# Performance work log

Hardware: AMD Instinct MI355X
Metric: run time of the kernel (lower is better)

Reference implementation:

```python
import jax, jax.numpy as jnp
import numpy as np

D = 400   # d_model
H = 16    # num heads
KD = 400  # keras MHA key_dim (per-head dim)
GU = 1800 # GRU units
EPS = 1e-6


def _ln(x, g, b):
    m = jnp.mean(x, -1, keepdims=True)
    v = jnp.mean((x - m) ** 2, -1, keepdims=True)
    return (x - m) * jax.lax.rsqrt(v + EPS) * g + b


def _gru_step(x, K, RK, B):
    # Single timestep keras GRU (reset_after=True, activation=elu, h0=0).
    h0 = jnp.zeros((x.shape[0], RK.shape[0]), x.dtype)
    xz, xr, xh = jnp.split(x @ K + B[0], 3, axis=-1)
    rz, rr, rh = jnp.split(h0 @ RK + B[1], 3, axis=-1)
    z = jax.nn.sigmoid(xz + rz)
    r = jax.nn.sigmoid(xr + rr)
    hh = jax.nn.elu(xh + r * rh)
    return z * h0 + (1.0 - z) * hh


def _forward(x, Wq, bq, Wk, bk, Wv, bv, Wo, bo, ln1_g, ln1_b,
             ffn_w1, ffn_b1, ffn_w2, ffn_b2, ln2_g, ln2_b,
             gru_fk, gru_frk, gru_fb, gru_bk, gru_brk, gru_bb,
             d2_w, d2_b, d4_w, d4_b, out_w, out_b):
    # The original python loop over growing prefixes is equivalent to one
    # batched encoder pass over inputs[1:, -1:, :] (seq_len==1, so MHA is
    # per-batch-element independent), with the raw row inputs[0] prepended.
    xe = x[1:, -1:, :]  # [N-1, 1, D]
    q = jnp.einsum('bsd,dhk->bshk', xe, Wq) + bq
    k = jnp.einsum('bsd,dhk->bshk', xe, Wk) + bk
    v = jnp.einsum('bsd,dhk->bshk', xe, Wv) + bv
    logits = jnp.einsum('bqhk,bmhk->bhqm', q, k) / jnp.sqrt(jnp.float32(KD))
    probs = jax.nn.softmax(logits, axis=-1)  # trivially ones (seq=1)
    ctx = jnp.einsum('bhqm,bmhk->bqhk', probs, v)
    attn = jnp.einsum('bqhk,hkd->bqd', ctx, Wo) + bo
    out1 = _ln(xe + attn, ln1_g, ln1_b)
    ffn = jax.nn.relu(out1 @ ffn_w1 + ffn_b1) @ ffn_w2 + ffn_b2
    enc = _ln(out1 + ffn, ln2_g, ln2_b)  # [N-1, 1, D]
    output = jnp.concatenate([x[:1, -1:, :], enc], axis=0)  # [N, 1, D]
    upd = jnp.concatenate([x, output], axis=1)              # [N, 4, D]
    flat = upd.reshape(x.shape[0], -1)                      # [N, 1600]
    # frozen cite_cos_sim_model (inference: dropout layers are identity)
    hf = _gru_step(flat, gru_fk, gru_frk, gru_fb)
    hb = _gru_step(flat, gru_bk, gru_brk, gru_bb)
    x1 = jnp.concatenate([hf, hb], axis=-1)   # [N, 3600]
    x3 = jax.nn.elu(x1 @ d2_w + d2_b)         # [N, 1800]
    x5 = jax.nn.elu(x3 @ d4_w + d4_b)         # [N, 1800]
    cat = jnp.concatenate([x1, x3, x5], axis=-1)  # [N, 7200]
    return cat @ out_w + out_b                # [N, 140]


def setup_inputs() -> dict:
    key = jax.random.key(0)
    shapes = {
        'Wq': (D, H, KD), 'bq': (H, KD), 'Wk': (D, H, KD), 'bk': (H, KD),
        'Wv': (D, H, KD), 'bv': (H, KD), 'Wo': (H, KD, D), 'bo': (D,),
        'ln1_b': (D,), 'ffn_w1': (D, 2), 'ffn_b1': (2,), 'ffn_w2': (2, D),
        'ffn_b2': (D,), 'ln2_b': (D,),
        'gru_fk': (1600, 3 * GU), 'gru_frk': (GU, 3 * GU), 'gru_fb': (2, 3 * GU),
        'gru_bk': (1600, 3 * GU), 'gru_brk': (GU, 3 * GU), 'gru_bb': (2, 3 * GU),
        'd2_w': (2 * GU, GU), 'd2_b': (GU,), 'd4_w': (GU, GU), 'd4_b': (GU,),
        'out_w': (4 * GU, 140), 'out_b': (140,),
    }
    keys = jax.random.split(key, len(shapes) + 1)
    inp = {'x': jax.random.normal(keys[0], (16384, 3, D), jnp.float32)}
    for i, (name, sh) in enumerate(shapes.items()):
        inp[name] = jax.random.normal(keys[i + 1], sh, jnp.float32) * 0.02
    inp['ln1_g'] = jnp.ones((D,), jnp.float32)
    inp['ln2_g'] = jnp.ones((D,), jnp.float32)
    return inp


def reference(x, Wq, bq, Wk, bk, Wv, bv, Wo, bo, ln1_g, ln1_b,
              ffn_w1, ffn_b1, ffn_w2, ffn_b2, ln2_g, ln2_b,
              gru_fk, gru_frk, gru_fb, gru_bk, gru_brk, gru_bb,
              d2_w, d2_b, d4_w, d4_b, out_w, out_b):
    return _forward(x, Wq, bq, Wk, bk, Wv, bv, Wo, bo, ln1_g, ln1_b,
                    ffn_w1, ffn_b1, ffn_w2, ffn_b2, ln2_g, ln2_b,
                    gru_fk, gru_frk, gru_fb, gru_bk, gru_brk, gru_bb,
                    d2_w, d2_b, d4_w, d4_b, out_w, out_b)
```

## Files before the change

### kernel.cpp

```cpp
#include <hip/hip_runtime.h>
#include <hip/hip_bf16.h>

typedef unsigned short u16;
using bf16x8 = __attribute__((ext_vector_type(8))) short;
using f32x4  = __attribute__((ext_vector_type(4))) float;

#define CM 2048
#define NC 8

#define P_LN1G 0
#define P_LN1B 400
#define P_FW1  800
#define P_FB1  1600
#define P_FW2  1602
#define P_FB2  2402
#define P_LN2G 2802
#define P_LN2B 3202
#define P_GFB  3602
#define P_GBB  14402
#define P_BV   25202
#define P_BO   31602
#define P_OB   32002
#define P_END  32142

__device__ __forceinline__ u16 f2bf(float f) {
  unsigned u = __float_as_uint(f);
  unsigned r = u + 0x7FFFu + ((u >> 16) & 1u);
  return (u16)(r >> 16);
}
__device__ __forceinline__ float bf2f(u16 h) {
  return __uint_as_float(((unsigned)h) << 16);
}

__device__ __forceinline__ void gl_lds16(const u16* g, u16* l) {
  __builtin_amdgcn_global_load_lds(
      (__attribute__((address_space(1))) void*)g,
      (__attribute__((address_space(3))) void*)l, 16, 0, 0);
}

__global__ void detect_dtype(int* flag, const void* x) {
  if (threadIdx.x == 0 && blockIdx.x == 0) {
    const u16* p = (const u16*)x;
    int cnt = 0;
    for (int i = 0; i < 64; i++) {
      int e = (p[2 * i] >> 7) & 0xFF;
      if (e >= 0x70 && e <= 0x85) cnt++;
    }
    *flag = (cnt >= 32) ? 1 : 0;
  }
}

__global__ void canon_bf(u16* __restrict__ dst, const void* __restrict__ src,
                         int n, const int* __restrict__ flag) {
  int i = blockIdx.x * 256 + threadIdx.x;
  if (i >= n) return;
  dst[i] = (*flag) ? ((const u16*)src)[i] : f2bf(((const float*)src)[i]);
}

__global__ void canon_x_rows(u16* __restrict__ dst, const void* __restrict__ src,
                             long base, int n, const int* __restrict__ flag) {
  int i = blockIdx.x * 256 + threadIdx.x;
  if (i >= n) return;
  long j = base + i;
  dst[i] = (*flag) ? ((const u16*)src)[j] : f2bf(((const float*)src)[j]);
}

__global__ void canon_f32k(float* __restrict__ dst, const void* __restrict__ src,
                           int n, const int* __restrict__ flag) {
  int i = blockIdx.x * 256 + threadIdx.x;
  if (i >= n) return;
  dst[i] = (*flag) ? bf2f(((const u16*)src)[i]) : ((const float*)src)[i];
}

__global__ void f32_to_bf(u16* __restrict__ dst, const float* __restrict__ src, int n) {
  int i = blockIdx.x * 256 + threadIdx.x;
  if (i < n) dst[i] = f2bf(src[i]);
}

template <int EPI, bool CL>
__global__ __launch_bounds__(256) void gemm_bt(
    const u16* __restrict__ A, const u16* __restrict__ Bt, void* __restrict__ Cv,
    const float* __restrict__ bias, int M, int N, int K, int lda, int ldb, int ldc,
    const u16* aend)
{
  __shared__ u16 lsA[128 * 32];
  __shared__ u16 lsB[128 * 32];
  const int tid = threadIdx.x;
  const int m0 = blockIdx.x * 128, n0 = blockIdx.y * 128;
  const int wave = tid >> 6, lane = tid & 63;
  const int wm = (wave >> 1) << 6, wn = (wave & 1) << 6;
  const int quad = lane >> 4, l16 = lane & 15;

  int ra = m0 + (tid >> 2);       if (ra > M - 1) ra = M - 1;
  int ra2 = m0 + 64 + (tid >> 2); if (ra2 > M - 1) ra2 = M - 1;
  int rb = n0 + (tid >> 2);       if (rb > N - 1) rb = N - 1;
  int rb2 = n0 + 64 + (tid >> 2); if (rb2 > N - 1) rb2 = N - 1;
  const u16* Ag  = A + (size_t)ra * lda + (tid & 3) * 8;
  const u16* Ag2 = A + (size_t)ra2 * lda + (tid & 3) * 8;
  const u16* Bg  = Bt + (size_t)rb * ldb + (tid & 3) * 8;
  const u16* Bg2 = Bt + (size_t)rb2 * ldb + (tid & 3) * 8;
  u16* la = lsA + tid * 8;
  u16* lb = lsB + tid * 8;

  f32x4 acc[4][4];
#pragma unroll
  for (int i = 0; i < 4; i++)
#pragma unroll
    for (int j = 0; j < 4; j++) acc[i][j] = (f32x4){0.f, 0.f, 0.f, 0.f};

  for (int k0 = 0; k0 < K; k0 += 32) {
    __syncthreads();
    const u16* pa  = Ag + k0;
    const u16* pa2 = Ag2 + k0;
    if (CL) { if (pa > aend) pa = aend; if (pa2 > aend) pa2 = aend; }
    gl_lds16(pa, la);
    gl_lds16(pa2, la + 2048);
    gl_lds16(Bg + k0, lb);
    gl_lds16(Bg2 + k0, lb + 2048);
    __syncthreads();
    bf16x8 af[4], bfv[4];
#pragma unroll
    for (int t = 0; t < 4; t++) {
      af[t]  = *(const bf16x8*)(lsA + ((wm + t * 16 + l16) << 5) + (quad << 3));
      bfv[t] = *(const bf16x8*)(lsB + ((wn + t * 16 + l16) << 5) + (quad << 3));
    }
#pragma unroll
    for (int mt = 0; mt < 4; mt++)
#pragma unroll
      for (int nt = 0; nt < 4; nt++)
        acc[mt][nt] = __builtin_amdgcn_mfma_f32_16x16x32_bf16(af[mt], bfv[nt], acc[mt][nt], 0, 0, 0);
  }

#pragma unroll
  for (int mt = 0; mt < 4; mt++)
#pragma unroll
    for (int r = 0; r < 4; r++) {
      const int row = m0 + wm + mt * 16 + quad * 4 + r;
      if (row < M) {
#pragma unroll
        for (int nt = 0; nt < 4; nt++) {
          const int col = n0 + wn + nt * 16 + l16;
          if (col < N) {
            float v = acc[mt][nt][r];
            if (EPI == 0) ((u16*)Cv)[(size_t)row * ldc + col] = f2bf(v);
            if (EPI == 1) ((float*)Cv)[(size_t)row * ldc + col] = v + bias[col];
            if (EPI == 2) {
              float p = v + bias[col];
              ((u16*)Cv)[(size_t)row * ldc + col] = f2bf(p > 0.f ? p : expm1f(p));
            }
          }
        }
      }
    }
}

template <int EPI>
__global__ __launch_bounds__(512, 2) void gemm256_bt(
    const u16* __restrict__ A, const u16* __restrict__ Bt, void* __restrict__ Cv,
    const float* __restrict__ bias, int M, int N, int K, int lda, int ldb, int ldc)
{
  __shared__ u16 lds8[65536];
  const int tid = threadIdx.x;
  const int m0 = blockIdx.x * 256, n0 = blockIdx.y * 256;
  const int wave = tid >> 6, lane = tid & 63;
  const int wm = (wave >> 2) * 128;
  const int wn = (wave & 3) * 64;
  const int quad = lane >> 4, l16 = lane & 15;

  const int srow = tid >> 3;
  const int sblk = ((tid & 7) ^ (srow & 7)) * 8;
  const u16* Ag[4];
  const u16* Bg[4];
#pragma unroll
  for (int i = 0; i < 4; i++) {
    int raw = m0 + i * 64 + srow; if (raw > M - 1) raw = M - 1;
    int rbw = n0 + i * 64 + srow; if (rbw > N - 1) rbw = N - 1;
    Ag[i] = A  + (size_t)raw * lda + sblk;
    Bg[i] = Bt + (size_t)rbw * ldb + sblk;
  }

  f32x4 acc[8][4];
#pragma unroll
  for (int i = 0; i < 8; i++)
#pragma unroll
    for (int j = 0; j < 4; j++) acc[i][j] = (f32x4){0.f, 0.f, 0.f, 0.f};

  const int nT = K >> 6;
#pragma unroll
  for (int i = 0; i < 4; i++) gl_lds16(Ag[i], lds8 + i * 4096 + tid * 8);
#pragma unroll
  for (int i = 0; i < 4; i++) gl_lds16(Bg[i], lds8 + 16384 + i * 4096 + tid * 8);

  int c = 0;
  for (int t = 0; t < nT; ++t) {
    __builtin_amdgcn_s_barrier();
    if (t + 1 < nT) {
      const int k1 = (t + 1) << 6;
      u16* dst = lds8 + (c ^ 1) * 32768;
#pragma unroll
      for (int i = 0; i < 4; i++) gl_lds16(Ag[i] + k1, dst + i * 4096 + tid * 8);
#pragma unroll
      for (int i = 0; i < 4; i++) gl_lds16(Bg[i] + k1, dst + 16384 + i * 4096 + tid * 8);
      asm volatile("s_waitcnt vmcnt(8)" ::: "memory");
    } else {
      asm volatile("s_waitcnt vmcnt(0)" ::: "memory");
    }
    __builtin_amdgcn_s_barrier();
    const u16* lA = lds8 + c * 32768;
    const u16* lB = lA + 16384;
#pragma unroll
    for (int kk = 0; kk < 2; kk++) {
      const int ch = kk * 4 + quad;
      bf16x8 af[8], bv[4];
#pragma unroll
      for (int mt = 0; mt < 8; mt++)
        af[mt] = *(const bf16x8*)(lA + (wm + mt * 16 + l16) * 64 + ((ch ^ (l16 & 7)) * 8));
#pragma unroll
      for (int nt = 0; nt < 4; nt++)
        bv[nt] = *(const bf16x8*)(lB + (wn + nt * 16 + l16) * 64 + ((ch ^ (l16 & 7)) * 8));
      __builtin_amdgcn_s_setprio(1);
#pragma unroll
      for (int mt = 0; mt < 8; mt++)
#pragma unroll
        for (int nt = 0; nt < 4; nt++)
          acc[mt][nt] = __builtin_amdgcn_mfma_f32_16x16x32_bf16(af[mt], bv[nt], acc[mt][nt], 0, 0, 0);
      __builtin_amdgcn_s_setprio(0);
    }
    c ^= 1;
  }

#pragma unroll
  for (int mt = 0; mt < 8; mt++)
#pragma unroll
    for (int r = 0; r < 4; r++) {
      const int row = m0 + wm + mt * 16 + quad * 4 + r;
      if (row < M) {
#pragma unroll
        for (int nt = 0; nt < 4; nt++) {
          const int col = n0 + wn + nt * 16 + l16;
          if (col < N) {
            float v = acc[mt][nt][r];
            if (EPI == 0) ((u16*)Cv)[(size_t)row * ldc + col] = f2bf(v);
            if (EPI == 2) {
              float p = v + bias[col];
              ((u16*)Cv)[(size_t)row * ldc + col] = f2bf(p > 0.f ? p : expm1f(p));
            }
          }
        }
      }
    }
}

__global__ __launch_bounds__(256) void gemm_bt_sk(
    const u16* __restrict__ A, const u16* __restrict__ Bt, float* __restrict__ outf,
    int M, int N, int K, int lda, int ldb, int ldc)
{
  __shared__ u16 lsA[128 * 32];
  __shared__ u16 lsB[128 * 32];
  const int tid = threadIdx.x;
  const int m0 = blockIdx.x * 128, n0 = blockIdx.y * 128;
  const int wave = tid >> 6, lane = tid & 63;
  const int wm = (wave >> 1) << 6, wn = (wave & 1) << 6;
  const int quad = lane >> 4, l16 = lane & 15;
  const int S = K >> 5, kz = blockIdx.z, KS = gridDim.z;
  const int s0 = (S * kz) / KS, s1 = (S * (kz + 1)) / KS;

  int ra = m0 + (tid >> 2);       if (ra > M - 1) ra = M - 1;
  int ra2 = m0 + 64 + (tid >> 2); if (ra2 > M - 1) ra2 = M - 1;
  int rb = n0 + (tid >> 2);       if (rb > N - 1) rb = N - 1;
  int rb2 = n0 + 64 + (tid >> 2); if (rb2 > N - 1) rb2 = N - 1;
  const u16* Ag  = A + (size_t)ra * lda + (tid & 3) * 8;
  const u16* Ag2 = A + (size_t)ra2 * lda + (tid & 3) * 8;
  const u16* Bg  = Bt + (size_t)rb * ldb + (tid & 3) * 8;
  const u16* Bg2 = Bt + (size_t)rb2 * ldb + (tid & 3) * 8;
  u16* la = lsA + tid * 8;
  u16* lb = lsB + tid * 8;

  f32x4 acc[4][4];
#pragma unroll
  for (int i = 0; i < 4; i++)
#pragma unroll
    for (int j = 0; j < 4; j++) acc[i][j] = (f32x4){0.f, 0.f, 0.f, 0.f};

  for (int s = s0; s < s1; ++s) {
    const int k0 = s << 5;
    __syncthreads();
    gl_lds16(Ag + k0, la);
    gl_lds16(Ag2 + k0, la + 2048);
    gl_lds16(Bg + k0, lb);
    gl_lds16(Bg2 + k0, lb + 2048);
    __syncthreads();
    bf16x8 af[4], bfv[4];
#pragma unroll
    for (int t = 0; t < 4; t++) {
      af[t]  = *(const bf16x8*)(lsA + ((wm + t * 16 + l16) << 5) + (quad << 3));
      bfv[t] = *(const bf16x8*)(lsB + ((wn + t * 16 + l16) << 5) + (quad << 3));
    }
#pragma unroll
    for (int mt = 0; mt < 4; mt++)
#pragma unroll
      for (int nt = 0; nt < 4; nt++)
        acc[mt][nt] = __builtin_amdgcn_mfma_f32_16x16x32_bf16(af[mt], bfv[nt], acc[mt][nt], 0, 0, 0);
  }

#pragma unroll
  for (int mt = 0; mt < 4; mt++)
#pragma unroll
    for (int r = 0; r < 4; r++) {
      const int row = m0 + wm + mt * 16 + quad * 4 + r;
      if (row < M) {
#pragma unroll
        for (int nt = 0; nt < 4; nt++) {
          const int col = n0 + wn + nt * 16 + l16;
          if (col < N) atomicAdd(&outf[(size_t)row * ldc + col], acc[mt][nt][r]);
        }
      }
    }
}

__global__ __launch_bounds__(256) void transpose_bf(
    u16* __restrict__ dst, const void* __restrict__ src, int SR, int SC, int DR, int DC,
    const int* __restrict__ flag)
{
  __shared__ u16 t[32][33];
  const int fl = *flag;
  const int tx = threadIdx.x & 31, ty = threadIdx.x >> 5;
  const int j0 = blockIdx.x << 5;
  const int i0 = blockIdx.y << 5;
#pragma unroll
  for (int s = 0; s < 32; s += 8) {
    int sr = j0 + ty + s, sc = i0 + tx;
    u16 v = 0;
    if (sr < SR && sc < SC) {
      size_t idx = (size_t)sr * SC + sc;
      v = fl ? ((const u16*)src)[idx] : f2bf(((const float*)src)[idx]);
    }
    t[ty + s][tx] = v;
  }
  __syncthreads();
#pragma unroll
  for (int s = 0; s < 32; s += 8) {
    int dr = i0 + ty + s, dc = j0 + tx;
    if (dr < DR && dc < DC) dst[(size_t)dr * DC + dc] = t[tx][ty + s];
  }
}

__global__ void build_outT(u16* __restrict__ dst, const void* __restrict__ ow,
                           const int* __restrict__ flag) {
  const int fl = *flag;
  int idx = blockIdx.x * 256 + threadIdx.x;
  if (idx >= 140 * 7264) return;
  int o = idx / 7264, c = idx - o * 7264;
  long si = -1;
  if (c < 3600) si = (long)c * 140 + o;
  else if (c >= 3616 && c < 5416) si = (long)(c - 16) * 140 + o;
  else if (c >= 5440 && c < 7240) si = (long)(c - 40) * 140 + o;
  u16 v = 0;
  if (si >= 0) v = fl ? ((const u16*)ow)[si] : f2bf(((const float*)ow)[si]);
  dst[idx] = v;
}

__global__ void zero_u32(unsigned* p, int n) {
  int i = blockIdx.x * 256 + threadIdx.x;
  if (i < n) p[i] = 0;
}

__global__ void zero_catpads(u16* cat, int rows) {
  int idx = blockIdx.x * 256 + threadIdx.x;
  if (idx >= rows * 64) return;
  int b = idx >> 6, t = idx & 63;
  int col = t < 16 ? 3600 + t : (t < 40 ? 5400 + t : 7200 + t);
  cat[(size_t)b * 7264 + col] = 0;
}

__global__ void init_outf(float* __restrict__ outf, const u16* __restrict__ pbuf) {
  int i = blockIdx.x * 256 + threadIdx.x;
  if (i < 16384 * 140) outf[i] = bf2f(pbuf[P_OB + i % 140]);
}

__device__ __forceinline__ void block_sum2(float& a, float& b, float* red, int t) {
#pragma unroll
  for (int o = 32; o > 0; o >>= 1) { a += __shfl_down(a, o, 64); b += __shfl_down(b, o, 64); }
  __syncthreads();
  if ((t & 63) == 0) { red[t >> 6] = a; red[4 + (t >> 6)] = b; }
  __syncthreads();
  a = red[0] + red[1] + red[2] + red[3];
  b = red[4] + red[5] + red[6] + red[7];
}

__global__ __launch_bounds__(256) void c0_kernel(float* c0, const u16* __restrict__ WoT,
                                                 const u16* __restrict__ pbuf) {
  __shared__ float red[8];
  int d = blockIdx.x, t = threadIdx.x;
  const u16* row = WoT + (size_t)d * 6400;
  const u16* bv = pbuf + P_BV;
  float s = 0.f;
  for (int j = t; j < 6400; j += 256) s += bf2f(bv[j]) * bf2f(row[j]);
  float dummy = 0.f;
  block_sum2(s, dummy, red, t);
  if (t == 0) c0[d] = s + bf2f(pbuf[P_BO + d]);
}

__global__ __launch_bounds__(256) void enc_rows(
    const u16* __restrict__ xc, const float* __restrict__ attn,
    const u16* __restrict__ pbuf, u16* __restrict__ flatc, int r0)
{
  __shared__ float red[8];
  const int li = blockIdx.x, t = threadIdx.x;
  const int gr = r0 + li;
  const u16* xr = xc + (size_t)li * 1200;
  u16* fr = flatc + (size_t)li * 1600;
  if (t < 150) ((uint4*)fr)[t] = ((const uint4*)xr)[t];
  if (gr == 0) {
    if (t < 50) ((uint4*)(fr + 1200))[t] = ((const uint4*)(xr + 800))[t];
    return;
  }
  const u16* xe = xr + 800;
  const float* at = attn + (size_t)li * 400;
  const u16 *g1 = pbuf + P_LN1G, *b1 = pbuf + P_LN1B, *fw1 = pbuf + P_FW1,
            *fb1v = pbuf + P_FB1, *fw2 = pbuf + P_FW2, *fb2v = pbuf + P_FB2,
            *g2 = pbuf + P_LN2G, *b2 = pbuf + P_LN2B;
  const int i1 = t + 256;
  float a0 = bf2f(xe[t]) + at[t];
  float a1 = 0.f;
  if (i1 < 400) a1 = bf2f(xe[i1]) + at[i1];
  float s = a0 + a1, ss = a0 * a0 + a1 * a1;
  block_sum2(s, ss, red, t);
  float mean = s * (1.f / 400.f);
  float var = ss * (1.f / 400.f) - mean * mean;
  float rstd = rsqrtf(var + 1e-6f);
  float o0 = (a0 - mean) * rstd * bf2f(g1[t]) + bf2f(b1[t]);
  float o1 = 0.f;
  if (i1 < 400) o1 = (a1 - mean) * rstd * bf2f(g1[i1]) + bf2f(b1[i1]);
  float d0 = o0 * bf2f(fw1[2 * t]), d1 = o0 * bf2f(fw1[2 * t + 1]);
  if (i1 < 400) { d0 += o1 * bf2f(fw1[2 * i1]); d1 += o1 * bf2f(fw1[2 * i1 + 1]); }
  block_sum2(d0, d1, red, t);
  float t0 = d0 + bf2f(fb1v[0]); t0 = t0 > 0.f ? t0 : 0.f;
  float t1 = d1 + bf2f(fb1v[1]); t1 = t1 > 0.f ? t1 : 0.f;
  float c0v = o0 + t0 * bf2f(fw2[t]) + t1 * bf2f(fw2[400 + t]) + bf2f(fb2v[t]);
  float c1v = 0.f;
  if (i1 < 400) c1v = o1 + t0 * bf2f(fw2[i1]) + t1 * bf2f(fw2[400 + i1]) + bf2f(fb2v[i1]);
  s = c0v + c1v; ss = c0v * c0v + c1v * c1v;
  block_sum2(s, ss, red, t);
  mean = s * (1.f / 400.f);
  var = ss * (1.f / 400.f) - mean * mean;
  rstd = rsqrtf(var + 1e-6f);
  u16* dr = fr + 1200;
  dr[t] = f2bf((c0v - mean) * rstd * bf2f(g2[t]) + bf2f(b2[t]));
  if (i1 < 400) dr[i1] = f2bf((c1v - mean) * rstd * bf2f(g2[i1]) + bf2f(b2[i1]));
}

__global__ __launch_bounds__(256) void gru_act(
    const u16* __restrict__ G, int ldg, const u16* __restrict__ pbuf, int boff,
    u16* __restrict__ cat, int off, int rows)
{
  int idx = blockIdx.x * 256 + threadIdx.x;
  if (idx >= rows * 1800) return;
  int b = idx / 1800, u = idx - b * 1800;
  const u16* g = G + (size_t)b * ldg;
  const u16* B = pbuf + boff;
  float xz = bf2f(g[u]) + bf2f(B[u]) + bf2f(B[5400 + u]);
  float xr = bf2f(g[1800 + u]) + bf2f(B[1800 + u]) + bf2f(B[7200 + u]);
  float xh = bf2f(g[3600 + u]) + bf2f(B[3600 + u]);
  float rh = bf2f(B[9000 + u]);
  float z = 1.f / (1.f + expf(-xz));
  float r = 1.f / (1.f + expf(-xr));
  float pre = xh + r * rh;
  float hh = pre > 0.f ? pre : expm1f(pre);
  cat[(size_t)b * 7264 + off + u] = f2bf((1.f - z) * hh);
}

extern "C" void kernel_launch(void* const* d_in, const int* in_sizes, int n_in,
                              void* d_out, int out_size, void* d_ws, size_t ws_size,
                              hipStream_t stream) {
  static const int MAP_DICT[22] = {5,6,7,8, 9,10,11,12,13,14, 15,17,18,20, 21,22,23,24, 25,26, 27,28};
  static const int MAP_SIG[22]  = {5,6,7,8, 10,11,12,13,14,16, 17,19,20,22, 23,24,25,26, 27,28, 9,15};
  const int* MAP = (in_sizes[15] > 100000) ? MAP_DICT : MAP_SIG;

  const void* x    = d_in[0];
  const void* Wv   = d_in[MAP[0]];
  const void* bv   = d_in[MAP[1]];
  const void* Wo   = d_in[MAP[2]];
  const void* bo   = d_in[MAP[3]];
  const void* ln1b = d_in[MAP[4]];
  const void* fw1  = d_in[MAP[5]];
  const void* fb1  = d_in[MAP[6]];
  const void* fw2  = d_in[MAP[7]];
  const void* fb2  = d_in[MAP[8]];
  const void* ln2b = d_in[MAP[9]];
  const void* gfk  = d_in[MAP[10]];
  const void* gfb  = d_in[MAP[11]];
  const void* gbk  = d_in[MAP[12]];
  const void* gbb  = d_in[MAP[13]];
  const void* d2w  = d_in[MAP[14]];
  const void* d2b  = d_in[MAP[15]];
  const void* d4w  = d_in[MAP[16]];
  const void* d4b  = d_in[MAP[17]];
  const void* ow   = d_in[MAP[18]];
  const void* ob   = d_in[MAP[19]];
  const void* ln1g = d_in[MAP[20]];
  const void* ln2g = d_in[MAP[21]];
  float* outf = (float*)d_out;

  unsigned char* base = (unsigned char*)d_ws;
  size_t off = 0;
  auto take = [&](size_t bytes) -> void* {
    void* p = base + off;
    off += (bytes + 255) & ~(size_t)255;
    return p;
  };
  u16*   KfT   = (u16*)take((size_t)5400 * 1600 * 2);
  u16*   KbT   = (u16*)take((size_t)5400 * 1600 * 2);
  u16*   d2T   = (u16*)take((size_t)1800 * 3616 * 2);
  u16*   d4T   = (u16*)take((size_t)1800 * 1824 * 2);
  u16*   outT  = (u16*)take((size_t)140 * 7264 * 2);
  u16*   WoT   = (u16*)take((size_t)400 * 6400 * 2);
  u16*   MT    = (u16*)take((size_t)400 * 416 * 2);
  float* MTf   = (float*)take((size_t)400 * 416 * 4);
  u16*   pbuf  = (u16*)take((size_t)P_END * 2);
  int*   flag  = (int*)take(256);
  float* c0    = (float*)take(400 * 4);
  float* d2bf  = (float*)take(1800 * 4);
  float* d4bf  = (float*)take(1800 * 4);

  int CMV = 0;
  {
    const size_t avail  = ws_size > off ? ws_size - off : 0;
    const size_t perrow = (size_t)(1600 + 10800 + 7264) * 2;
    const size_t margin = (size_t)4 << 20;
    if      (avail >= (size_t)16384 * perrow + margin) CMV = 16384;
    else if (avail >= (size_t)8192  * perrow + margin) CMV = 8192;
    else if (avail >= (size_t)4096  * perrow + margin) CMV = 4096;
    else if (avail >= (size_t)2048  * perrow + margin) CMV = 2048;
  }

  u16 *flatc, *Gc, *catc;
  if (CMV) {
    flatc = (u16*)take((size_t)CMV * 1600 * 2);
    Gc    = (u16*)take((size_t)CMV * 10800 * 2);
    catc  = (u16*)take((size_t)CMV * 7264 * 2);
  } else {
    flatc = (u16*)take((size_t)CM * 1600 * 2);
    Gc    = (u16*)take((size_t)CM * 5400 * 2);
    catc  = (u16*)take((size_t)CM * 7264 * 2);
  }
  const int rows = CMV ? CMV : CM;
  float* attnc = (float*)Gc;
  u16*   xc    = (u16*)((unsigned char*)Gc + (size_t)rows * 1600);
  u16*   Wvc   = catc;

  detect_dtype<<<1, 64, 0, stream>>>(flag, x);
  canon_bf<<<2, 256, 0, stream>>>(pbuf + P_LN1G, ln1g, 400, flag);
  canon_bf<<<2, 256, 0, stream>>>(pbuf + P_LN1B, ln1b, 400, flag);
  canon_bf<<<4, 256, 0, stream>>>(pbuf + P_FW1, fw1, 800, flag);
  canon_bf<<<1, 256, 0, stream>>>(pbuf + P_FB1, fb1, 2, flag);
  canon_bf<<<4, 256, 0, stream>>>(pbuf + P_FW2, fw2, 800, flag);
  canon_bf<<<2, 256, 0, stream>>>(pbuf + P_FB2, fb2, 400, flag);
  canon_bf<<<2, 256, 0, stream>>>(pbuf + P_LN2G, ln2g, 400, flag);
  canon_bf<<<2, 256, 0, stream>>>(pbuf + P_LN2B, ln2b, 400, flag);
  canon_bf<<<43, 256, 0, stream>>>(pbuf + P_GFB, gfb, 10800, flag);
  canon_bf<<<43, 256, 0, stream>>>(pbuf + P_GBB, gbb, 10800, flag);
  canon_bf<<<25, 256, 0, stream>>>(pbuf + P_BV, bv, 6400, flag);
  canon_bf<<<2, 256, 0, stream>>>(pbuf + P_BO, bo, 400, flag);
  canon_bf<<<1, 256, 0, stream>>>(pbuf + P_OB, ob, 140, flag);
  canon_f32k<<<8, 256, 0, stream>>>(d2bf, d2b, 1800, flag);
  canon_f32k<<<8, 256, 0, stream>>>(d4bf, d4b, 1800, flag);

  transpose_bf<<<dim3(50, 169), 256, 0, stream>>>(KfT, gfk, 1600, 5400, 5400, 1600, flag);
  transpose_bf<<<dim3(50, 169), 256, 0, stream>>>(KbT, gbk, 1600, 5400, 5400, 1600, flag);
  transpose_bf<<<dim3(113, 57), 256, 0, stream>>>(d2T, d2w, 3600, 1800, 1800, 3616, flag);
  transpose_bf<<<dim3(57, 57), 256, 0, stream>>>(d4T, d4w, 1800, 1800, 1800, 1824, flag);
  transpose_bf<<<dim3(200, 13), 256, 0, stream>>>(WoT, Wo, 6400, 400, 400, 6400, flag);
  build_outT<<<(140 * 7264 + 255) / 256, 256, 0, stream>>>(outT, ow, flag);
  init_outf<<<(16384 * 140 + 255) / 256, 256, 0, stream>>>(outf, pbuf);
  c0_kernel<<<400, 256, 0, stream>>>(c0, WoT, pbuf);

  canon_bf<<<10000, 256, 0, stream>>>(Wvc, Wv, 2560000, flag);
  zero_u32<<<(166400 + 255) / 256, 256, 0, stream>>>((unsigned*)MTf, 166400);
  gemm_bt_sk<<<dim3(4, 4, 16), 256, 0, stream>>>(WoT, Wvc, MTf,
      400, 400, 6400, 6400, 6400, 416);
  f32_to_bf<<<(166400 + 255) / 256, 256, 0, stream>>>(MT, MTf, 166400);

  if (CMV) {
    zero_catpads<<<(CMV * 64 + 255) / 256, 256, 0, stream>>>(catc, CMV);
    const int nchunk = 16384 / CMV;
    for (int c = 0; c < nchunk; ++c) {
      const long r0 = (long)c * CMV;
      canon_x_rows<<<(CMV * 1200 + 255) / 256, 256, 0, stream>>>(
          xc, x, r0 * 1200, CMV * 1200, flag);
      gemm_bt<1, true><<<dim3(CMV / 128, 4), 256, 0, stream>>>(
          xc + 800, MT, attnc, c0, CMV, 400, 416, 1200, 416, 400,
          xc + (size_t)CMV * 1200 - 8);
      enc_rows<<<CMV, 256, 0, stream>>>(xc, attnc, pbuf, flatc, (int)r0);
      gemm256_bt<0><<<dim3(CMV / 256, 43), 512, 0, stream>>>(
          flatc, KfT, Gc, nullptr, CMV, 10800, 1600, 1600, 1600, 10800);
      gru_act<<<(CMV * 1800 + 255) / 256, 256, 0, stream>>>(
          Gc, 10800, pbuf, P_GFB, catc, 0, CMV);
      gru_act<<<(CMV * 1800 + 255) / 256, 256, 0, stream>>>(
          Gc + 5400, 10800, pbuf, P_GBB, catc, 1800, CMV);
      gemm_bt<2, false><<<dim3(CMV / 128, 15), 256, 0, stream>>>(
          catc, d2T, catc + 3616, d2bf, CMV, 1800, 3616, 7264, 3616, 7264, nullptr);
      gemm_bt<2, false><<<dim3(CMV / 128, 15), 256, 0, stream>>>(
          catc + 3616, d4T, catc + 5440, d4bf, CMV, 1800, 1824, 7264, 1824, 7264, nullptr);
      gemm_bt_sk<<<dim3(CMV / 128, 2, 8), 256, 0, stream>>>(
          catc, outT, outf + (size_t)r0 * 140, CMV, 140, 7264, 7264, 7264, 140);
    }
  } else {
    zero_catpads<<<(CM * 64 + 255) / 256, 256, 0, stream>>>(catc, CM);
    for (int c = 0; c < NC; ++c) {
      const int r0 = c * CM;
      canon_x_rows<<<(CM * 1200 + 255) / 256, 256, 0, stream>>>(
          xc, x, (long)r0 * 1200, CM * 1200, flag);
      gemm_bt<1, true><<<dim3(CM / 128, 4), 256, 0, stream>>>(
          xc + 800, MT, attnc, c0, CM, 400, 416, 1200, 416, 400,
          xc + (size_t)CM * 1200 - 8);
      enc_rows<<<CM, 256, 0, stream>>>(xc, attnc, pbuf, flatc, r0);
      gemm_bt<0, false><<<dim3(CM / 128, 43), 256, 0, stream>>>(
          flatc, KfT, Gc, nullptr, CM, 5400, 1600, 1600, 1600, 5400, nullptr);
      gru_act<<<(CM * 1800 + 255) / 256, 256, 0, stream>>>(
          Gc, 5400, pbuf, P_GFB, catc, 0, CM);
      gemm_bt<0, false><<<dim3(CM / 128, 43), 256, 0, stream>>>(
          flatc, KbT, Gc, nullptr, CM, 5400, 1600, 1600, 1600, 5400, nullptr);
      gru_act<<<(CM * 1800 + 255) / 256, 256, 0, stream>>>(
          Gc, 5400, pbuf, P_GBB, catc, 1800, CM);
      gemm_bt<2, false><<<dim3(CM / 128, 15), 256, 0, stream>>>(
          catc, d2T, catc + 3616, d2bf, CM, 1800, 3616, 7264, 3616, 7264, nullptr);
      gemm_bt<2, false><<<dim3(CM / 128, 15), 256, 0, stream>>>(
          catc + 3616, d4T, catc + 5440, d4bf, CM, 1800, 1824, 7264, 1824, 7264, nullptr);
      gemm_bt_sk<<<dim3(CM / 128, 2, 8), 256, 0, stream>>>(
          catc, outT, outf + (size_t)r0 * 140, CM, 140, 7264, 7264, 7264, 140);
    }
  }
}
```

Baseline: 2.282 ms.

## Deepen GEMM256 pipeline to 4 stages, split-K attention GEMM, fuse GRU activations

The 256x256 GEMM now uses K-tiles of 32 with a four-buffer LDS ring and three tiles prefetched ahead, in place of 64-wide double buffering. The goal is to hide more global-load latency behind MFMA work. The attention projection GEMM becomes a split-K atomic kernel that writes into a bias-initialised fp32 buffer, adding parallelism for that narrow output. The forward and backward GRU activation kernels are merged into a single launch. In exchange there are more barriers per K, an extra init kernel, and atomic accumulation.

```diff
diff --git a/kernel.cpp b/kernel.cpp
--- a/kernel.cpp
+++ b/kernel.cpp
@@ -77,6 +77,12 @@
   if (i < n) dst[i] = f2bf(src[i]);
 }
 
+__global__ void init_bias_f32(float* __restrict__ dst, const float* __restrict__ b,
+                              int p, int n) {
+  int i = blockIdx.x * 256 + threadIdx.x;
+  if (i < n) dst[i] = b[i % p];
+}
+
 template <int EPI, bool CL>
 __global__ __launch_bounds__(256) void gemm_bt(
     const u16* __restrict__ A, const u16* __restrict__ Bt, void* __restrict__ Cv,
@@ -167,14 +173,14 @@
   const int wn = (wave & 3) * 64;
   const int quad = lane >> 4, l16 = lane & 15;
 
-  const int srow = tid >> 3;
-  const int sblk = ((tid & 7) ^ (srow & 7)) * 8;
-  const u16* Ag[4];
-  const u16* Bg[4];
-#pragma unroll
-  for (int i = 0; i < 4; i++) {
-    int raw = m0 + i * 64 + srow; if (raw > M - 1) raw = M - 1;
-    int rbw = n0 + i * 64 + srow; if (rbw > N - 1) rbw = N - 1;
+  const int srow = tid >> 2;
+  const int sblk = ((tid & 3) ^ ((srow >> 1) & 3)) * 8;
+  const u16* Ag[2];
+  const u16* Bg[2];
+#pragma unroll
+  for (int i = 0; i < 2; i++) {
+    int raw = m0 + i * 128 + srow; if (raw > M - 1) raw = M - 1;
+    int rbw = n0 + i * 128 + srow; if (rbw > N - 1) rbw = N - 1;
     Ag[i] = A  + (size_t)raw * lda + sblk;
     Bg[i] = Bt + (size_t)rbw * ldb + sblk;
   }
@@ -185,48 +191,58 @@
 #pragma unroll
     for (int j = 0; j < 4; j++) acc[i][j] = (f32x4){0.f, 0.f, 0.f, 0.f};
 
-  const int nT = K >> 6;
-#pragma unroll
-  for (int i = 0; i < 4; i++) gl_lds16(Ag[i], lds8 + i * 4096 + tid * 8);
-#pragma unroll
-  for (int i = 0; i < 4; i++) gl_lds16(Bg[i], lds8 + 16384 + i * 4096 + tid * 8);
-
-  int c = 0;
+  const int nT = K >> 5;
+#pragma unroll
+  for (int p = 0; p < 3; ++p) {
+    if (p < nT) {
+      u16* dst = lds8 + p * 16384;
+      const int kp = p << 5;
+#pragma unroll
+      for (int i = 0; i < 2; i++) gl_lds16(Ag[i] + kp, dst + i * 4096 + tid * 8);
+#pragma unroll
+      for (int i = 0; i < 2; i++) gl_lds16(Bg[i] + kp, dst + 8192 + i * 4096 + tid * 8);
+    }
+  }
+
   for (int t = 0; t < nT; ++t) {
     __builtin_amdgcn_s_barrier();
-    if (t + 1 < nT) {
-      const int k1 = (t + 1) << 6;
-      u16* dst = lds8 + (c ^ 1) * 32768;
-#pragma unroll
-      for (int i = 0; i < 4; i++) gl_lds16(Ag[i] + k1, dst + i * 4096 + tid * 8);
-#pragma unroll
-      for (int i = 0; i < 4; i++) gl_lds16(Bg[i] + k1, dst + 16384 + i * 4096 + tid * 8);
+    if (t + 3 < nT) {
+      const int k1 = (t + 3) << 5;
+      u16* dst = lds8 + ((t + 3) & 3) * 16384;
+#pragma unroll
+      for (int i = 0; i < 2; i++) gl_lds16(Ag[i] + k1, dst + i * 4096 + tid * 8);
+#pragma unroll
+      for (int i = 0; i < 2; i++) gl_lds16(Bg[i] + k1, dst + 8192 + i * 4096 + tid * 8);
+      asm volatile("s_waitcnt vmcnt(12)" ::: "memory");
+    } else if (t + 2 < nT) {
       asm volatile("s_waitcnt vmcnt(8)" ::: "memory");
+    } else if (t + 1 < nT) {
+      asm volatile("s_waitcnt vmcnt(4)" ::: "memory");
     } else {
       asm volatile("s_waitcnt vmcnt(0)" ::: "memory");
     }
     __builtin_amdgcn_s_barrier();
-    const u16* lA = lds8 + c * 32768;
-    const u16* lB = lA + 16384;
-#pragma unroll
-    for (int kk = 0; kk < 2; kk++) {
-      const int ch = kk * 4 + quad;
-      bf16x8 af[8], bv[4];
-#pragma unroll
-      for (int mt = 0; mt < 8; mt++)
-        af[mt] = *(const bf16x8*)(lA + (wm + mt * 16 + l16) * 64 + ((ch ^ (l16 & 7)) * 8));
+
+    const u16* lA = lds8 + (t & 3) * 16384;
+    const u16* lB = lA + 8192;
+    bf16x8 av[8], bv[4];
+#pragma unroll
+    for (int mt = 0; mt < 8; mt++) {
+      const int row = wm + mt * 16 + l16;
+      av[mt] = *(const bf16x8*)(lA + row * 32 + ((quad ^ ((row >> 1) & 3)) * 8));
+    }
+#pragma unroll
+    for (int nt = 0; nt < 4; nt++) {
+      const int row = wn + nt * 16 + l16;
+      bv[nt] = *(const bf16x8*)(lB + row * 32 + ((quad ^ ((row >> 1) & 3)) * 8));
+    }
+    __builtin_amdgcn_s_setprio(1);
+#pragma unroll
+    for (int mt = 0; mt < 8; mt++)
 #pragma unroll
       for (int nt = 0; nt < 4; nt++)
-        bv[nt] = *(const bf16x8*)(lB + (wn + nt * 16 + l16) * 64 + ((ch ^ (l16 & 7)) * 8));
-      __builtin_amdgcn_s_setprio(1);
-#pragma unroll
-      for (int mt = 0; mt < 8; mt++)
-#pragma unroll
-        for (int nt = 0; nt < 4; nt++)
-          acc[mt][nt] = __builtin_amdgcn_mfma_f32_16x16x32_bf16(af[mt], bv[nt], acc[mt][nt], 0, 0, 0);
-      __builtin_amdgcn_s_setprio(0);
-    }
-    c ^= 1;
+        acc[mt][nt] = __builtin_amdgcn_mfma_f32_16x16x32_bf16(av[mt], bv[nt], acc[mt][nt], 0, 0, 0);
+    __builtin_amdgcn_s_setprio(0);
   }
 
 #pragma unroll
@@ -251,9 +267,10 @@
     }
 }
 
+template <bool CL>
 __global__ __launch_bounds__(256) void gemm_bt_sk(
     const u16* __restrict__ A, const u16* __restrict__ Bt, float* __restrict__ outf,
-    int M, int N, int K, int lda, int ldb, int ldc)
+    int M, int N, int K, int lda, int ldb, int ldc, const u16* aend)
 {
   __shared__ u16 lsA[128 * 32];
   __shared__ u16 lsB[128 * 32];
@@ -285,8 +302,11 @@
   for (int s = s0; s < s1; ++s) {
     const int k0 = s << 5;
     __syncthreads();
-    gl_lds16(Ag + k0, la);
-    gl_lds16(Ag2 + k0, la + 2048);
+    const u16* pa  = Ag + k0;
+    const u16* pa2 = Ag2 + k0;
+    if (CL) { if (pa > aend) pa = aend; if (pa2 > aend) pa2 = aend; }
+    gl_lds16(pa, la);
+    gl_lds16(pa2, la + 2048);
     gl_lds16(Bg + k0, lb);
     gl_lds16(Bg2 + k0, lb + 2048);
     __syncthreads();
@@ -470,6 +490,28 @@
   cat[(size_t)b * 7264 + off + u] = f2bf((1.f - z) * hh);
 }
 
+__global__ __launch_bounds__(256) void gru_act2(
+    const u16* __restrict__ G, const u16* __restrict__ pbuf,
+    u16* __restrict__ cat, int rows)
+{
+  int idx = blockIdx.x * 256 + threadIdx.x;
+  if (idx >= rows * 3600) return;
+  int b = idx / 3600, u2 = idx - b * 3600;
+  const int fwd = u2 < 1800;
+  const int u = fwd ? u2 : u2 - 1800;
+  const u16* g = G + (size_t)b * 10800 + (fwd ? 0 : 5400);
+  const u16* B = pbuf + (fwd ? P_GFB : P_GBB);
+  float xz = bf2f(g[u]) + bf2f(B[u]) + bf2f(B[5400 + u]);
+  float xr = bf2f(g[1800 + u]) + bf2f(B[1800 + u]) + bf2f(B[7200 + u]);
+  float xh = bf2f(g[3600 + u]) + bf2f(B[3600 + u]);
+  float rh = bf2f(B[9000 + u]);
+  float z = 1.f / (1.f + expf(-xz));
+  float r = 1.f / (1.f + expf(-xr));
+  float pre = xh + r * rh;
+  float hh = pre > 0.f ? pre : expm1f(pre);
+  cat[(size_t)b * 7264 + u2] = f2bf((1.f - z) * hh);
+}
+
 extern "C" void kernel_launch(void* const* d_in, const int* in_sizes, int n_in,
                               void* d_out, int out_size, void* d_ws, size_t ws_size,
                               hipStream_t stream) {
@@ -577,8 +619,8 @@
 
   canon_bf<<<10000, 256, 0, stream>>>(Wvc, Wv, 2560000, flag);
   zero_u32<<<(166400 + 255) / 256, 256, 0, stream>>>((unsigned*)MTf, 166400);
-  gemm_bt_sk<<<dim3(4, 4, 16), 256, 0, stream>>>(WoT, Wvc, MTf,
-      400, 400, 6400, 6400, 6400, 416);
+  gemm_bt_sk<false><<<dim3(4, 4, 16), 256, 0, stream>>>(WoT, Wvc, MTf,
+      400, 400, 6400, 6400, 6400, 416, nullptr);
   f32_to_bf<<<(166400 + 255) / 256, 256, 0, stream>>>(MT, MTf, 166400);
 
   if (CMV) {
@@ -588,22 +630,20 @@
       const long r0 = (long)c * CMV;
       canon_x_rows<<<(CMV * 1200 + 255) / 256, 256, 0, stream>>>(
           xc, x, r0 * 1200, CMV * 1200, flag);
-      gemm_bt<1, true><<<dim3(CMV / 128, 4), 256, 0, stream>>>(
-          xc + 800, MT, attnc, c0, CMV, 400, 416, 1200, 416, 400,
+      init_bias_f32<<<(CMV * 400 + 255) / 256, 256, 0, stream>>>(attnc, c0, 400, CMV * 400);
+      gemm_bt_sk<true><<<dim3(CMV / 128, 4, 4), 256, 0, stream>>>(
+          xc + 800, MT, attnc, CMV, 400, 416, 1200, 416, 400,
           xc + (size_t)CMV * 1200 - 8);
       enc_rows<<<CMV, 256, 0, stream>>>(xc, attnc, pbuf, flatc, (int)r0);
       gemm256_bt<0><<<dim3(CMV / 256, 43), 512, 0, stream>>>(
           flatc, KfT, Gc, nullptr, CMV, 10800, 1600, 1600, 1600, 10800);
-      gru_act<<<(CMV * 1800 + 255) / 256, 256, 0, stream>>>(
-          Gc, 10800, pbuf, P_GFB, catc, 0, CMV);
-      gru_act<<<(CMV * 1800 + 255) / 256, 256, 0, stream>>>(
-          Gc + 5400, 10800, pbuf, P_GBB, catc, 1800, CMV);
+      gru_act2<<<(CMV * 3600 + 255) / 256, 256, 0, stream>>>(Gc, pbuf, catc, CMV);
       gemm_bt<2, false><<<dim3(CMV / 128, 15), 256, 0, stream>>>(
           catc, d2T, catc + 3616, d2bf, CMV, 1800, 3616, 7264, 3616, 7264, nullptr);
       gemm_bt<2, false><<<dim3(CMV / 128, 15), 256, 0, stream>>>(
           catc + 3616, d4T, catc + 5440, d4bf, CMV, 1800, 1824, 7264, 1824, 7264, nullptr);
-      gemm_bt_sk<<<dim3(CMV / 128, 2, 8), 256, 0, stream>>>(
-          catc, outT, outf + (size_t)r0 * 140, CMV, 140, 7264, 7264, 7264, 140);
+      gemm_bt_sk<false><<<dim3(CMV / 128, 2, 8), 256, 0, stream>>>(
+          catc, outT, outf + (size_t)r0 * 140, CMV, 140, 7264, 7264, 7264, 140, nullptr);
     }
   } else {
     zero_catpads<<<(CM * 64 + 255) / 256, 256, 0, stream>>>(catc, CM);
@@ -627,8 +667,8 @@
           catc, d2T, catc + 3616, d2bf, CM, 1800, 3616, 7264, 3616, 7264, nullptr);
       gemm_bt<2, false><<<dim3(CM / 128, 15), 256, 0, stream>>>(
           catc + 3616, d4T, catc + 5440, d4bf, CM, 1800, 1824, 7264, 1824, 7264, nullptr);
-      gemm_bt_sk<<<dim3(CM / 128, 2, 8), 256, 0, stream>>>(
-          catc, outT, outf + (size_t)r0 * 140, CM, 140, 7264, 7264, 7264, 140);
-    }
-  }
-}
+      gemm_bt_sk<false><<<dim3(CM / 128, 2, 8), 256, 0, stream>>>(
+          catc, outT, outf + (size_t)r0 * 140, CM, 140, 7264, 7264, 7264, 140, nullptr);
+    }
+  }
+}
```

New measurement: 2.331 ms. 2.2% more time.
